# Optimization experiments

Measured on AMD Instinct MI355X. Metric: run time of the kernel, lower is better.

## Reference

```python
import jax, jax.numpy as jnp
import numpy as np

B, N, C = 2, 30, 320
FH = FW = 64          # feature map (latent 128 / downsample 2)
PH = PW = 32          # roi_scale output size at this level
ORIG = 128.0          # original (latent) spatial size
SCALE = 0.5           # spatial_scale = 1/downsample_rate
SR = 2                # sampling_ratio
M = N + 1             # global channel + rois


def _bilinear(img, y, x):
    # img: (C, H, W); y, x: arbitrary-shape float coords. torchvision-style:
    # zero outside [-1, H]/[ -1, W], clamp then 4-corner interp.
    H, W = img.shape[1], img.shape[2]
    valid = (y > -1.0) & (y < H) & (x > -1.0) & (x < W)
    yc = jnp.clip(y, 0.0, H - 1.0)
    xc = jnp.clip(x, 0.0, W - 1.0)
    y0 = jnp.floor(yc).astype(jnp.int32)
    x0 = jnp.floor(xc).astype(jnp.int32)
    y1 = jnp.minimum(y0 + 1, H - 1)
    x1 = jnp.minimum(x0 + 1, W - 1)
    wy = yc - y0
    wx = xc - x0
    v = (img[:, y0, x0] * (1 - wy) * (1 - wx)
         + img[:, y0, x1] * (1 - wy) * wx
         + img[:, y1, x0] * wy * (1 - wx)
         + img[:, y1, x1] * wy * wx)
    return v * valid


def _roi_align_one(img, x1, y1, bw, bh):
    # img (C,FH,FW); x1,y1,bw,bh (N,) in aligned feature coords / bin sizes
    s = (jnp.arange(PH * SR, dtype=img.dtype) + 0.5) / SR   # sub-sample offsets in bin units
    yy = y1[:, None] + s[None, :] * bh[:, None]             # (N, PH*SR)
    xx = x1[:, None] + s[None, :] * bw[:, None]             # (N, PW*SR)
    yg = jnp.broadcast_to(yy[:, :, None], (N, PH * SR, PW * SR))
    xg = jnp.broadcast_to(xx[:, None, :], (N, PH * SR, PW * SR))
    v = _bilinear(img, yg, xg)                              # (C, N, PH*SR, PW*SR)
    v = v.reshape(C, N, PH, SR, PW, SR).mean(axis=(3, 5))   # average sub-samples
    return v.transpose(1, 0, 2, 3)                          # (N, C, PH, PW)


def _roi_unpool_one(roi_imgs, x1, y1, bw, bh):
    # inverse of roi_align: paste each (C,PH,PW) roi back into its own (FH,FW) map
    ys = jnp.arange(FH, dtype=roi_imgs.dtype)
    xs = jnp.arange(FW, dtype=roi_imgs.dtype)
    ry = (ys[None, :] - y1[:, None]) / bh[:, None] - 0.5    # (N, FH) roi-grid coords
    rx = (xs[None, :] - x1[:, None]) / bw[:, None] - 0.5    # (N, FW)
    ryg = jnp.broadcast_to(ry[:, :, None], (N, FH, FW))
    rxg = jnp.broadcast_to(rx[:, None, :], (N, FH, FW))
    return jax.vmap(_bilinear)(roi_imgs, ryg, rxg)          # (N, C, FH, FW); zeros outside box


def _fuser(x, perm, w_reduce, w1, b1, w2, b2):
    # FuseWeightGenerator: x (B, M, C, H, W)
    fg = jnp.sum(x, axis=2) != 0                            # (B, M, H, W) foreground mask
    fw = jnp.einsum('bmchw,c->bmhw', x, w_reduce)           # 1x1 conv C->1, no bias
    g = fw[:, :1]
    r = fw[:, 1:][:, perm]                                  # shuffle roi channels
    gin = jnp.concatenate([g, r], axis=1)                   # (B, M, H, W)
    # ChannelGate: only the 'max' branch affects the output (original uses last channel_att_raw)
    mp = gin.max(axis=(2, 3))                               # (B, M)
    att = jax.nn.relu(mp @ w1 + b1) @ w2 + b2
    gated = gin * jax.nn.sigmoid(att)[:, :, None, None]
    inv = jnp.argsort(perm)
    fw = jnp.concatenate([gated[:, :1], gated[:, 1:][:, inv]], axis=1)
    fw = jnp.where(fg, fw, jnp.finfo(fw.dtype).min)
    w = jax.nn.softmax(fw, axis=1)[:, :, None]              # (B, M, 1, H, W)
    return jnp.sum(x * w, axis=1)                           # (B, C, H, W)


def _forward(normed_hidden_states, attn_output, instance_boxes, instance_masks, perm,
             w_reduce, w1, b1, w2, b2):
    fmap = normed_hidden_states.reshape(B, FH, FW, C).transpose(0, 3, 1, 2)  # b c h w
    boxes = instance_boxes * ORIG * SCALE - 0.5             # aligned=True feature coords
    x1, y1 = boxes[..., 0], boxes[..., 1]
    x2, y2 = boxes[..., 2], boxes[..., 3]
    bw = (x2 - x1) / PW
    bh = (y2 - y1) / PH
    roi_feats = jax.vmap(_roi_align_one)(fmap, x1, y1, bw, bh)   # (B,N,C,PH,PW)
    mask = instance_masks.astype(roi_feats.dtype)[:, :, None, None, None]
    roi_feats = roi_feats * mask                             # masked rois stay zero
    unpooled = jax.vmap(_roi_unpool_one)(roi_feats, x1, y1, bw, bh) * mask  # (B,N,C,FH,FW)
    attn_map = attn_output.reshape(B, FH, FW, C).transpose(0, 3, 1, 2)[:, None]
    x = jnp.concatenate([attn_map, unpooled], axis=1)        # (B, M, C, FH, FW)
    fused = _fuser(x, perm, w_reduce, w1, b1, w2, b2)        # (B, C, FH, FW)
    return fused.transpose(0, 2, 3, 1).reshape(B, FH * FW, C)


def setup_inputs() -> dict:
    key = jax.random.key(0)
    ks = jax.random.split(key, 10)
    nhs = jax.random.normal(ks[0], (B, FH * FW, C), dtype=jnp.float32)
    attn = jax.random.normal(ks[1], (B, FH * FW, C), dtype=jnp.float32)
    cx = jax.random.uniform(ks[2], (B, N), minval=0.25, maxval=0.75)
    cy = jax.random.uniform(ks[3], (B, N), minval=0.25, maxval=0.75)
    hw = jax.random.uniform(ks[4], (B, N, 2), minval=0.1, maxval=0.4)
    boxes = jnp.stack([cx - hw[..., 0] / 2, cy - hw[..., 1] / 2,
                       cx + hw[..., 0] / 2, cy + hw[..., 1] / 2], axis=-1)
    boxes = jnp.clip(boxes, 0.0, 1.0).astype(jnp.float32)    # normalized xyxy
    masks = jax.random.randint(ks[5], (B, N), 0, 2).astype(jnp.int32)
    perm = jax.random.permutation(ks[6], N).astype(jnp.int32)
    w_reduce = (jax.random.normal(ks[7], (C,), dtype=jnp.float32) / np.sqrt(C)).astype(jnp.float32)
    w1 = (jax.random.normal(ks[8], (M, M), dtype=jnp.float32) / np.sqrt(M)).astype(jnp.float32)
    b1 = jnp.zeros((M,), dtype=jnp.float32)
    w2 = (jax.random.normal(ks[9], (M, M), dtype=jnp.float32) / np.sqrt(M)).astype(jnp.float32)
    b2 = jnp.zeros((M,), dtype=jnp.float32)
    return {"normed_hidden_states": nhs, "attn_output": attn, "instance_boxes": boxes,
            "instance_masks": masks, "perm": perm, "w_reduce": w_reduce,
            "w1": w1, "b1": b1, "w2": w2, "b2": b2}


def reference(normed_hidden_states, attn_output, instance_boxes, instance_masks, perm,
              w_reduce, w1, b1, w2, b2):
    return _forward(normed_hidden_states, attn_output, instance_boxes, instance_masks, perm,
                    w_reduce, w1, b1, w2, b2)
```

## Files before the change

kernel.cpp:

```cpp
#include <hip/hip_runtime.h>
#include <hip/hip_bf16.h>

#define NB 2
#define NN 30
#define NC 320
#define NM 31
#define HW 4096
#define FMIN_F (-3.40282346638528859812e+38f)

typedef float nfloat4 __attribute__((ext_vector_type(4)));

#define OFF_FSUM   0
#define OFF_FWRED  8192
#define OFF_ASUM   16384
#define OFF_AWRED  24576
#define OFF_Z      32768
#define OFF_MP     286720
#define WS_FLOATS  286784

#define GRID_ROIF (NB * NN * 256)
#define GRID_RED  1639

__device__ __forceinline__ void get_box(const float* boxes, int b, int n,
                                        float& x1, float& y1, float& bw, float& bh) {
    const float* p = boxes + (b * NN + n) * 4;
    float X1 = p[0] * 64.0f - 0.5f;
    float Y1 = p[1] * 64.0f - 0.5f;
    float X2 = p[2] * 64.0f - 0.5f;
    float Y2 = p[3] * 64.0f - 0.5f;
    x1 = X1; y1 = Y1;
    bw = (X2 - X1) / 32.0f;
    bh = (Y2 - Y1) / 32.0f;
}

__device__ __forceinline__ unsigned short f2bf(float f) {
    __hip_bfloat16 h = __float2bfloat16(f);
    return *reinterpret_cast<unsigned short*>(&h);
}
__device__ __forceinline__ float bf2f(unsigned short u) {
    return __uint_as_float(((unsigned int)u) << 16);
}

__device__ void do_roifeat(int blk, const float* __restrict__ nhs,
                           const float* __restrict__ boxes,
                           const int* __restrict__ masks,
                           unsigned short* __restrict__ roif) {
    int bn = blk >> 8;
    int n = bn % NN;
    int b = bn / NN;
    if (masks[b * NN + n] == 0) return;
    int tid = threadIdx.x;
    int cid = tid / 80;
    int v = tid - cid * 80;
    int cell = blk * 4 + cid;
    int q = cell & 31;
    int p = (cell >> 5) & 31;
    float x1, y1, bw, bh;
    get_box(boxes, b, n, x1, y1, bw, bh);
    float wc[4][4];
    int ic[4][4];
    bool vv[4];
#pragma unroll
    for (int s_ = 0; s_ < 4; s_++) {
        int di = s_ >> 1, dj = s_ & 1;
        float y = y1 + ((float)p + 0.25f + 0.5f * (float)di) * bh;
        float x = x1 + ((float)q + 0.25f + 0.5f * (float)dj) * bw;
        vv[s_] = (y > -1.0f) && (y < 64.0f) && (x > -1.0f) && (x < 64.0f);
        float yc = fminf(fmaxf(y, 0.0f), 63.0f);
        float xc = fminf(fmaxf(x, 0.0f), 63.0f);
        int iy0 = (int)floorf(yc), ix0 = (int)floorf(xc);
        int iy1 = min(iy0 + 1, 63), ix1 = min(ix0 + 1, 63);
        float wy = yc - (float)iy0, wx = xc - (float)ix0;
        wc[s_][0] = (1.f - wy) * (1.f - wx);
        wc[s_][1] = (1.f - wy) * wx;
        wc[s_][2] = wy * (1.f - wx);
        wc[s_][3] = wy * wx;
        ic[s_][0] = iy0 * 64 + ix0;
        ic[s_][1] = iy0 * 64 + ix1;
        ic[s_][2] = iy1 * 64 + ix0;
        ic[s_][3] = iy1 * 64 + ix1;
    }
    const float4* fb4 = (const float4*)(nhs + (size_t)b * HW * NC);
    float4 acc = make_float4(0.f, 0.f, 0.f, 0.f);
#pragma unroll
    for (int s_ = 0; s_ < 4; s_++) {
        if (vv[s_]) {
#pragma unroll
            for (int t_ = 0; t_ < 4; t_++) {
                float w = wc[s_][t_];
                float4 fv = fb4[ic[s_][t_] * 80 + v];
                acc.x += w * fv.x; acc.y += w * fv.y;
                acc.z += w * fv.z; acc.w += w * fv.w;
            }
        }
    }
    ushort4 pk;
    pk.x = f2bf(acc.x * 0.25f);
    pk.y = f2bf(acc.y * 0.25f);
    pk.z = f2bf(acc.z * 0.25f);
    pk.w = f2bf(acc.w * 0.25f);
    ((ushort4*)roif)[(size_t)cell * 80 + v] = pk;
}

__device__ void do_reduce(int rblk, const float* __restrict__ nhs,
                          const float* __restrict__ attn,
                          const float* __restrict__ wred, float* __restrict__ ws) {
    int wave = threadIdx.x >> 6;
    int lane = threadIdx.x & 63;
    int row = rblk * 5 + wave;
    if (row >= NB * HW) return;
    const float4* n4 = (const float4*)(nhs + (size_t)row * NC);
    const float4* a4 = (const float4*)(attn + (size_t)row * NC);
    const float4* w4 = (const float4*)wred;
    float4 wv = w4[lane];
    float4 nv = n4[lane];
    float4 av = a4[lane];
    float s_n = nv.x + nv.y + nv.z + nv.w;
    float w_n = nv.x * wv.x + nv.y * wv.y + nv.z * wv.z + nv.w * wv.w;
    float s_a = av.x + av.y + av.z + av.w;
    float w_a = av.x * wv.x + av.y * wv.y + av.z * wv.z + av.w * wv.w;
    if (lane < 16) {
        float4 wv2 = w4[lane + 64];
        float4 nv2 = n4[lane + 64];
        float4 av2 = a4[lane + 64];
        s_n += nv2.x + nv2.y + nv2.z + nv2.w;
        w_n += nv2.x * wv2.x + nv2.y * wv2.y + nv2.z * wv2.z + nv2.w * wv2.w;
        s_a += av2.x + av2.y + av2.z + av2.w;
        w_a += av2.x * wv2.x + av2.y * wv2.y + av2.z * wv2.z + av2.w * wv2.w;
    }
#pragma unroll
    for (int off = 32; off > 0; off >>= 1) {
        s_n += __shfl_down(s_n, off, 64);
        w_n += __shfl_down(w_n, off, 64);
        s_a += __shfl_down(s_a, off, 64);
        w_a += __shfl_down(w_a, off, 64);
    }
    if (lane == 0) {
        ws[OFF_FSUM + row]  = s_n;
        ws[OFF_FWRED + row] = w_n;
        ws[OFF_ASUM + row]  = s_a;
        ws[OFF_AWRED + row] = w_a;
    }
}

__global__ void k_stage1(const float* __restrict__ nhs, const float* __restrict__ attn,
                         const float* __restrict__ boxes, const int* __restrict__ masks,
                         const float* __restrict__ wred, float* __restrict__ ws,
                         unsigned short* __restrict__ roif) {
    int blk = blockIdx.x;
    if (blk < GRID_ROIF) {
        do_roifeat(blk, nhs, boxes, masks, roif);
    } else {
        do_reduce(blk - GRID_ROIF, nhs, attn, wred, ws);
    }
}

__global__ void k_fw(const float* __restrict__ boxes, const int* __restrict__ masks,
                     float* __restrict__ ws) {
    int bm = blockIdx.x;
    int b = bm / NM, m = bm % NM;
    __shared__ float rs[1024], rw[1024];
    __shared__ float red[256];
    float locmax = -INFINITY;
    int tid = threadIdx.x;
    if (m == 0) {
        for (int pix = tid; pix < HW; pix += 256) {
            float fwv = ws[OFF_AWRED + b * HW + pix];
            bool fg = (ws[OFF_ASUM + b * HW + pix] != 0.0f);
            ws[OFF_Z + (size_t)bm * HW + pix] = fg ? fwv : FMIN_F;
            locmax = fmaxf(locmax, fwv);
        }
    } else {
        int n = m - 1;
        int msk = masks[b * NN + n];
        if (msk) {
            float x1, y1, bw, bh;
            get_box(boxes, b, n, x1, y1, bw, bh);
            const float* fsum  = ws + OFF_FSUM + b * HW;
            const float* fwred = ws + OFF_FWRED + b * HW;
            for (int cell = tid; cell < 1024; cell += 256) {
                int q = cell & 31, p = cell >> 5;
                float accs = 0.f, accw = 0.f;
#pragma unroll
                for (int di = 0; di < 2; di++) {
#pragma unroll
                    for (int dj = 0; dj < 2; dj++) {
                        float y = y1 + ((float)p + 0.25f + 0.5f * (float)di) * bh;
                        float x = x1 + ((float)q + 0.25f + 0.5f * (float)dj) * bw;
                        bool valid = (y > -1.0f) && (y < 64.0f) && (x > -1.0f) && (x < 64.0f);
                        if (valid) {
                            float yc = fminf(fmaxf(y, 0.0f), 63.0f);
                            float xc = fminf(fmaxf(x, 0.0f), 63.0f);
                            int iy0 = (int)floorf(yc), ix0 = (int)floorf(xc);
                            int iy1 = min(iy0 + 1, 63), ix1 = min(ix0 + 1, 63);
                            float wy = yc - (float)iy0, wx = xc - (float)ix0;
                            float w00 = (1.f - wy) * (1.f - wx), w01 = (1.f - wy) * wx;
                            float w10 = wy * (1.f - wx), w11 = wy * wx;
                            accs += w00 * fsum[iy0 * 64 + ix0] + w01 * fsum[iy0 * 64 + ix1]
                                  + w10 * fsum[iy1 * 64 + ix0] + w11 * fsum[iy1 * 64 + ix1];
                            accw += w00 * fwred[iy0 * 64 + ix0] + w01 * fwred[iy0 * 64 + ix1]
                                  + w10 * fwred[iy1 * 64 + ix0] + w11 * fwred[iy1 * 64 + ix1];
                        }
                    }
                }
                rs[cell] = accs * 0.25f;
                rw[cell] = accw * 0.25f;
            }
            __syncthreads();
            for (int pix = tid; pix < HW; pix += 256) {
                int h = pix >> 6, wp = pix & 63;
                float fwv = 0.0f;
                bool fg = false;
                float ry = ((float)h - y1) / bh - 0.5f;
                float rx = ((float)wp - x1) / bw - 0.5f;
                bool valid = (ry > -1.0f) && (ry < 32.0f) && (rx > -1.0f) && (rx < 32.0f);
                if (valid) {
                    float yc = fminf(fmaxf(ry, 0.0f), 31.0f);
                    float xc = fminf(fmaxf(rx, 0.0f), 31.0f);
                    int iy0 = (int)floorf(yc), ix0 = (int)floorf(xc);
                    int iy1 = min(iy0 + 1, 31), ix1 = min(ix0 + 1, 31);
                    float wy = yc - (float)iy0, wx = xc - (float)ix0;
                    float w00 = (1.f - wy) * (1.f - wx), w01 = (1.f - wy) * wx;
                    float w10 = wy * (1.f - wx), w11 = wy * wx;
                    fwv = w00 * rw[iy0 * 32 + ix0] + w01 * rw[iy0 * 32 + ix1]
                        + w10 * rw[iy1 * 32 + ix0] + w11 * rw[iy1 * 32 + ix1];
                    float su = w00 * rs[iy0 * 32 + ix0] + w01 * rs[iy0 * 32 + ix1]
                             + w10 * rs[iy1 * 32 + ix0] + w11 * rs[iy1 * 32 + ix1];
                    fg = (su != 0.0f);
                }
                ws[OFF_Z + (size_t)bm * HW + pix] = fg ? fwv : FMIN_F;
                locmax = fmaxf(locmax, fwv);
            }
        } else {
            for (int pix = tid; pix < HW; pix += 256)
                ws[OFF_Z + (size_t)bm * HW + pix] = FMIN_F;
            locmax = 0.0f;
        }
    }
    red[tid] = locmax;
    __syncthreads();
    for (int s = 128; s > 0; s >>= 1) {
        if (tid < s) red[tid] = fmaxf(red[tid], red[tid + s]);
        __syncthreads();
    }
    if (tid == 0) ws[OFF_MP + bm] = red[0];
}

__global__ void k_final(const float* __restrict__ attn, const float* __restrict__ boxes,
                        const int* __restrict__ perm, const float* __restrict__ w1,
                        const float* __restrict__ b1, const float* __restrict__ w2,
                        const float* __restrict__ b2, const float* __restrict__ ws,
                        const unsigned short* __restrict__ roif, float* __restrict__ out) {
    __shared__ float mpg[NM], hb[NM], scal[32], wbuf[4][32];
    int t = threadIdx.x;
    int idx0 = blockIdx.x * 4;
    int b = idx0 >> 12;

    if (t < NM) {
        mpg[t] = (t == 0) ? ws[OFF_MP + b * NM]
                          : ws[OFF_MP + b * NM + 1 + perm[t - 1]];
    }
    __syncthreads();
    if (t < NM) {
        float a = b1[t];
#pragma unroll
        for (int k = 0; k < NM; k++) a += mpg[k] * w1[k * NM + t];
        hb[t] = fmaxf(a, 0.0f);
    }
    __syncthreads();
    if (t < NM) {
        float a = b2[t];
#pragma unroll
        for (int k = 0; k < NM; k++) a += hb[k] * w2[k * NM + t];
        float sig = 1.0f / (1.0f + expf(-a));
        if (t == 0) scal[0] = sig;
        else        scal[1 + perm[t - 1]] = sig;
    }
    __syncthreads();

    if (t < 128) {
        int pg = t >> 5, m = t & 31;
        int pix = (idx0 + pg) & 4095;
        float zz = FMIN_F;
        if (m < NM) {
            float v = ws[OFF_Z + (size_t)(b * NM + m) * HW + pix];
            zz = (v == FMIN_F) ? FMIN_F : v * scal[m];
        }
        float mx = zz;
#pragma unroll
        for (int off = 16; off > 0; off >>= 1)
            mx = fmaxf(mx, __shfl_xor(mx, off, 64));
        float e = (m < NM) ? expf(zz - mx) : 0.0f;
        float s = e;
#pragma unroll
        for (int off = 16; off > 0; off >>= 1)
            s += __shfl_xor(s, off, 64);
        if (m < NM) wbuf[pg][m] = e / s;
    }
    __syncthreads();

    int pid = t / 80;
    int v = t - pid * 80;
    int idx = idx0 + pid;
    int pix = idx & 4095;
    int h = pix >> 6, wp = pix & 63;
    float w0 = wbuf[pid][0];
    float4 a4 = ((const float4*)attn)[(size_t)idx * 80 + v];
    float4 acc;
    acc.x = a4.x * w0; acc.y = a4.y * w0; acc.z = a4.z * w0; acc.w = a4.w * w0;
    const ushort4* r4 = (const ushort4*)roif;
    for (int n = 0; n < NN; n++) {
        float wn = wbuf[pid][n + 1];
        if (wn == 0.0f) continue;
        float x1, y1, bw, bh;
        get_box(boxes, b, n, x1, y1, bw, bh);
        float ry = ((float)h - y1) / bh - 0.5f;
        float rx = ((float)wp - x1) / bw - 0.5f;
        float yc = fminf(fmaxf(ry, 0.0f), 31.0f);
        float xc = fminf(fmaxf(rx, 0.0f), 31.0f);
        int iy0 = (int)floorf(yc), ix0 = (int)floorf(xc);
        int iy1 = min(iy0 + 1, 31), ix1 = min(ix0 + 1, 31);
        float wy = yc - (float)iy0, wx = xc - (float)ix0;
        float w00 = (1.f - wy) * (1.f - wx) * wn, w01 = (1.f - wy) * wx * wn;
        float w10 = wy * (1.f - wx) * wn, w11 = wy * wx * wn;
        size_t base = ((size_t)(b * NN + n)) << 10;
        ushort4 u00 = r4[(base + iy0 * 32 + ix0) * 80 + v];
        ushort4 u01 = r4[(base + iy0 * 32 + ix1) * 80 + v];
        ushort4 u10 = r4[(base + iy1 * 32 + ix0) * 80 + v];
        ushort4 u11 = r4[(base + iy1 * 32 + ix1) * 80 + v];
        acc.x += w00 * bf2f(u00.x) + w01 * bf2f(u01.x) + w10 * bf2f(u10.x) + w11 * bf2f(u11.x);
        acc.y += w00 * bf2f(u00.y) + w01 * bf2f(u01.y) + w10 * bf2f(u10.y) + w11 * bf2f(u11.y);
        acc.z += w00 * bf2f(u00.z) + w01 * bf2f(u01.z) + w10 * bf2f(u10.z) + w11 * bf2f(u11.z);
        acc.w += w00 * bf2f(u00.w) + w01 * bf2f(u01.w) + w10 * bf2f(u10.w) + w11 * bf2f(u11.w);
    }
    nfloat4 nv = { acc.x, acc.y, acc.z, acc.w };
    __builtin_nontemporal_store(nv, ((nfloat4*)out) + (size_t)idx * 80 + v);
}

extern "C" void kernel_launch(void* const* d_in, const int* in_sizes, int n_in,
                              void* d_out, int out_size, void* d_ws, size_t ws_size,
                              hipStream_t stream) {
    const float* nhs   = (const float*)d_in[0];
    const float* attn  = (const float*)d_in[1];
    const float* boxes = (const float*)d_in[2];
    const int*   masks = (const int*)d_in[3];
    const int*   perm  = (const int*)d_in[4];
    const float* wred  = (const float*)d_in[5];
    const float* w1    = (const float*)d_in[6];
    const float* b1    = (const float*)d_in[7];
    const float* w2    = (const float*)d_in[8];
    const float* b2    = (const float*)d_in[9];
    float* out = (float*)d_out;
    float* ws = (float*)d_ws;
    unsigned short* roif = (unsigned short*)((char*)d_ws + (size_t)WS_FLOATS * 4);

    k_stage1<<<GRID_ROIF + GRID_RED, 320, 0, stream>>>(nhs, attn, boxes, masks, wred, ws, roif);
    k_fw<<<NB * NM, 256, 0, stream>>>(boxes, masks, ws);
    k_final<<<NB * HW / 4, 320, 0, stream>>>(attn, boxes, perm, w1, b1, w2, b2, ws, roif, out);
}
```

Baseline: 131.6 us.

## Merge ROI-align subsample taps into a 3x3 footprint and widen per-thread vectors

ROI feature pooling now computes, once per cell in shared memory, a combined 3x3 weight stencil covering all four subsamples. Each cell's channels are then gathered once per distinct pixel instead of up to sixteen times. Both the ROI-feature pass and the final kernel now process 8 channels per thread using 128-bit bf16 packs, with 8 pixels per block, which halves the block count. The out-of-range validity checks are dropped in the ROI and k_fw sampling. This relies on boxes being clipped to [0,1] and on subsample spacing staying within one pixel.

```diff
diff --git a/kernel.cpp b/kernel.cpp
--- a/kernel.cpp
+++ b/kernel.cpp
@@ -18,7 +18,7 @@
 #define OFF_MP     286720
 #define WS_FLOATS  286784
 
-#define GRID_ROIF (NB * NN * 256)
+#define GRID_ROIF (NB * NN * 128)
 #define GRID_RED  1639
 
 __device__ __forceinline__ void get_box(const float* boxes, int b, int n,
@@ -37,69 +37,103 @@
     __hip_bfloat16 h = __float2bfloat16(f);
     return *reinterpret_cast<unsigned short*>(&h);
 }
-__device__ __forceinline__ float bf2f(unsigned short u) {
-    return __uint_as_float(((unsigned int)u) << 16);
-}
+__device__ __forceinline__ unsigned pack2(float a, float b) {
+    return (unsigned)f2bf(a) | ((unsigned)f2bf(b) << 16);
+}
+__device__ __forceinline__ float blo(unsigned u) { return __uint_as_float(u << 16); }
+__device__ __forceinline__ float bhi(unsigned u) { return __uint_as_float(u & 0xffff0000u); }
 
 __device__ void do_roifeat(int blk, const float* __restrict__ nhs,
                            const float* __restrict__ boxes,
                            const int* __restrict__ masks,
-                           unsigned short* __restrict__ roif) {
-    int bn = blk >> 8;
+                           unsigned* __restrict__ roif) {
+    int bn = blk >> 7;
     int n = bn % NN;
     int b = bn / NN;
     if (masks[b * NN + n] == 0) return;
+    __shared__ float wsm[8][9];
+    __shared__ int bsm[8];
     int tid = threadIdx.x;
-    int cid = tid / 80;
-    int v = tid - cid * 80;
-    int cell = blk * 4 + cid;
-    int q = cell & 31;
-    int p = (cell >> 5) & 31;
     float x1, y1, bw, bh;
     get_box(boxes, b, n, x1, y1, bw, bh);
-    float wc[4][4];
-    int ic[4][4];
-    bool vv[4];
-#pragma unroll
-    for (int s_ = 0; s_ < 4; s_++) {
-        int di = s_ >> 1, dj = s_ & 1;
-        float y = y1 + ((float)p + 0.25f + 0.5f * (float)di) * bh;
-        float x = x1 + ((float)q + 0.25f + 0.5f * (float)dj) * bw;
-        vv[s_] = (y > -1.0f) && (y < 64.0f) && (x > -1.0f) && (x < 64.0f);
-        float yc = fminf(fmaxf(y, 0.0f), 63.0f);
-        float xc = fminf(fmaxf(x, 0.0f), 63.0f);
-        int iy0 = (int)floorf(yc), ix0 = (int)floorf(xc);
-        int iy1 = min(iy0 + 1, 63), ix1 = min(ix0 + 1, 63);
-        float wy = yc - (float)iy0, wx = xc - (float)ix0;
-        wc[s_][0] = (1.f - wy) * (1.f - wx);
-        wc[s_][1] = (1.f - wy) * wx;
-        wc[s_][2] = wy * (1.f - wx);
-        wc[s_][3] = wy * wx;
-        ic[s_][0] = iy0 * 64 + ix0;
-        ic[s_][1] = iy0 * 64 + ix1;
-        ic[s_][2] = iy1 * 64 + ix0;
-        ic[s_][3] = iy1 * 64 + ix1;
-    }
+
+    if (tid < 8) {
+        int cell = blk * 8 + tid;
+        int q = cell & 31;
+        int p = (cell >> 5) & 31;
+        float W[9] = {0.f,0.f,0.f,0.f,0.f,0.f,0.f,0.f,0.f};
+        float wys[4], wxs[4];
+        int iy0s[4], ix0s[4];
+        int iymin = 64, ixmin = 64;
+#pragma unroll
+        for (int s_ = 0; s_ < 4; s_++) {
+            int di = s_ >> 1, dj = s_ & 1;
+            float y = y1 + ((float)p + 0.25f + 0.5f * (float)di) * bh;
+            float x = x1 + ((float)q + 0.25f + 0.5f * (float)dj) * bw;
+            float yc = fminf(fmaxf(y, 0.0f), 63.0f);
+            float xc = fminf(fmaxf(x, 0.0f), 63.0f);
+            int iy0 = (int)floorf(yc), ix0 = (int)floorf(xc);
+            wys[s_] = yc - (float)iy0;
+            wxs[s_] = xc - (float)ix0;
+            iy0s[s_] = iy0; ix0s[s_] = ix0;
+            iymin = min(iymin, iy0); ixmin = min(ixmin, ix0);
+        }
+#pragma unroll
+        for (int s_ = 0; s_ < 4; s_++) {
+            float wy = wys[s_], wx = wxs[s_];
+            int dy = iy0s[s_] - iymin;
+            int dx = ix0s[s_] - ixmin;
+            bool yt = (iy0s[s_] == 63);
+            bool xt = (ix0s[s_] == 63);
+            float ay0 = yt ? 1.0f : (1.0f - wy);
+            float ay1 = yt ? 0.0f : wy;
+            float ax0 = xt ? 1.0f : (1.0f - wx);
+            float ax1 = xt ? 0.0f : wx;
+            float r0 = dy ? 0.0f : ay0;
+            float r1 = dy ? ay0  : ay1;
+            float r2 = dy ? ay1  : 0.0f;
+            float c0 = dx ? 0.0f : ax0;
+            float c1 = dx ? ax0  : ax1;
+            float c2 = dx ? ax1  : 0.0f;
+            W[0] += r0 * c0; W[1] += r0 * c1; W[2] += r0 * c2;
+            W[3] += r1 * c0; W[4] += r1 * c1; W[5] += r1 * c2;
+            W[6] += r2 * c0; W[7] += r2 * c1; W[8] += r2 * c2;
+        }
+#pragma unroll
+        for (int k = 0; k < 9; k++) wsm[tid][k] = W[k] * 0.25f;
+        bsm[tid] = iymin * 64 + ixmin;
+    }
+    __syncthreads();
+
+    int cid = tid / 40;
+    int v = tid - cid * 40;
+    int cell = blk * 8 + cid;
     const float4* fb4 = (const float4*)(nhs + (size_t)b * HW * NC);
-    float4 acc = make_float4(0.f, 0.f, 0.f, 0.f);
-#pragma unroll
-    for (int s_ = 0; s_ < 4; s_++) {
-        if (vv[s_]) {
-#pragma unroll
-            for (int t_ = 0; t_ < 4; t_++) {
-                float w = wc[s_][t_];
-                float4 fv = fb4[ic[s_][t_] * 80 + v];
-                acc.x += w * fv.x; acc.y += w * fv.y;
-                acc.z += w * fv.z; acc.w += w * fv.w;
+    int base = bsm[cid];
+    float4 acc0 = make_float4(0.f, 0.f, 0.f, 0.f);
+    float4 acc1 = make_float4(0.f, 0.f, 0.f, 0.f);
+#pragma unroll
+    for (int i = 0; i < 3; i++) {
+#pragma unroll
+        for (int j = 0; j < 3; j++) {
+            float w = wsm[cid][i * 3 + j];
+            if (w != 0.0f) {
+                int off = (base + i * 64 + j) * 80 + v * 2;
+                float4 f0 = fb4[off];
+                float4 f1 = fb4[off + 1];
+                acc0.x += w * f0.x; acc0.y += w * f0.y;
+                acc0.z += w * f0.z; acc0.w += w * f0.w;
+                acc1.x += w * f1.x; acc1.y += w * f1.y;
+                acc1.z += w * f1.z; acc1.w += w * f1.w;
             }
         }
     }
-    ushort4 pk;
-    pk.x = f2bf(acc.x * 0.25f);
-    pk.y = f2bf(acc.y * 0.25f);
-    pk.z = f2bf(acc.z * 0.25f);
-    pk.w = f2bf(acc.w * 0.25f);
-    ((ushort4*)roif)[(size_t)cell * 80 + v] = pk;
+    uint4 pk;
+    pk.x = pack2(acc0.x, acc0.y);
+    pk.y = pack2(acc0.z, acc0.w);
+    pk.z = pack2(acc1.x, acc1.y);
+    pk.w = pack2(acc1.z, acc1.w);
+    ((uint4*)roif)[(size_t)cell * 40 + v] = pk;
 }
 
 __device__ void do_reduce(int rblk, const float* __restrict__ nhs,
@@ -146,7 +180,7 @@
 __global__ void k_stage1(const float* __restrict__ nhs, const float* __restrict__ attn,
                          const float* __restrict__ boxes, const int* __restrict__ masks,
                          const float* __restrict__ wred, float* __restrict__ ws,
-                         unsigned short* __restrict__ roif) {
+                         unsigned* __restrict__ roif) {
     int blk = blockIdx.x;
     if (blk < GRID_ROIF) {
         do_roifeat(blk, nhs, boxes, masks, roif);
@@ -187,20 +221,17 @@
                     for (int dj = 0; dj < 2; dj++) {
                         float y = y1 + ((float)p + 0.25f + 0.5f * (float)di) * bh;
                         float x = x1 + ((float)q + 0.25f + 0.5f * (float)dj) * bw;
-                        bool valid = (y > -1.0f) && (y < 64.0f) && (x > -1.0f) && (x < 64.0f);
-                        if (valid) {
-                            float yc = fminf(fmaxf(y, 0.0f), 63.0f);
-                            float xc = fminf(fmaxf(x, 0.0f), 63.0f);
-                            int iy0 = (int)floorf(yc), ix0 = (int)floorf(xc);
-                            int iy1 = min(iy0 + 1, 63), ix1 = min(ix0 + 1, 63);
-                            float wy = yc - (float)iy0, wx = xc - (float)ix0;
-                            float w00 = (1.f - wy) * (1.f - wx), w01 = (1.f - wy) * wx;
-                            float w10 = wy * (1.f - wx), w11 = wy * wx;
-                            accs += w00 * fsum[iy0 * 64 + ix0] + w01 * fsum[iy0 * 64 + ix1]
-                                  + w10 * fsum[iy1 * 64 + ix0] + w11 * fsum[iy1 * 64 + ix1];
-                            accw += w00 * fwred[iy0 * 64 + ix0] + w01 * fwred[iy0 * 64 + ix1]
-                                  + w10 * fwred[iy1 * 64 + ix0] + w11 * fwred[iy1 * 64 + ix1];
-                        }
+                        float yc = fminf(fmaxf(y, 0.0f), 63.0f);
+                        float xc = fminf(fmaxf(x, 0.0f), 63.0f);
+                        int iy0 = (int)floorf(yc), ix0 = (int)floorf(xc);
+                        int iy1 = min(iy0 + 1, 63), ix1 = min(ix0 + 1, 63);
+                        float wy = yc - (float)iy0, wx = xc - (float)ix0;
+                        float w00 = (1.f - wy) * (1.f - wx), w01 = (1.f - wy) * wx;
+                        float w10 = wy * (1.f - wx), w11 = wy * wx;
+                        accs += w00 * fsum[iy0 * 64 + ix0] + w01 * fsum[iy0 * 64 + ix1]
+                              + w10 * fsum[iy1 * 64 + ix0] + w11 * fsum[iy1 * 64 + ix1];
+                        accw += w00 * fwred[iy0 * 64 + ix0] + w01 * fwred[iy0 * 64 + ix1]
+                              + w10 * fwred[iy1 * 64 + ix0] + w11 * fwred[iy1 * 64 + ix1];
                     }
                 }
                 rs[cell] = accs * 0.25f;
@@ -250,10 +281,10 @@
                         const int* __restrict__ perm, const float* __restrict__ w1,
                         const float* __restrict__ b1, const float* __restrict__ w2,
                         const float* __restrict__ b2, const float* __restrict__ ws,
-                        const unsigned short* __restrict__ roif, float* __restrict__ out) {
-    __shared__ float mpg[NM], hb[NM], scal[32], wbuf[4][32];
+                        const unsigned* __restrict__ roif, float* __restrict__ out) {
+    __shared__ float mpg[NM], hb[NM], scal[32], wbuf[8][32];
     int t = threadIdx.x;
-    int idx0 = blockIdx.x * 4;
+    int idx0 = blockIdx.x * 8;
     int b = idx0 >> 12;
 
     if (t < NM) {
@@ -278,7 +309,7 @@
     }
     __syncthreads();
 
-    if (t < 128) {
+    if (t < 256) {
         int pg = t >> 5, m = t & 31;
         int pix = (idx0 + pg) & 4095;
         float zz = FMIN_F;
@@ -299,16 +330,19 @@
     }
     __syncthreads();
 
-    int pid = t / 80;
-    int v = t - pid * 80;
+    int pid = t / 40;
+    int v = t - pid * 40;
     int idx = idx0 + pid;
     int pix = idx & 4095;
     int h = pix >> 6, wp = pix & 63;
     float w0 = wbuf[pid][0];
-    float4 a4 = ((const float4*)attn)[(size_t)idx * 80 + v];
-    float4 acc;
-    acc.x = a4.x * w0; acc.y = a4.y * w0; acc.z = a4.z * w0; acc.w = a4.w * w0;
-    const ushort4* r4 = (const ushort4*)roif;
+    const float4* at4 = (const float4*)attn;
+    float4 a0 = at4[(size_t)idx * 80 + v * 2];
+    float4 a1 = at4[(size_t)idx * 80 + v * 2 + 1];
+    float4 acc0, acc1;
+    acc0.x = a0.x * w0; acc0.y = a0.y * w0; acc0.z = a0.z * w0; acc0.w = a0.w * w0;
+    acc1.x = a1.x * w0; acc1.y = a1.y * w0; acc1.z = a1.z * w0; acc1.w = a1.w * w0;
+    const uint4* r4 = (const uint4*)roif;
     for (int n = 0; n < NN; n++) {
         float wn = wbuf[pid][n + 1];
         if (wn == 0.0f) continue;
@@ -324,17 +358,23 @@
         float w00 = (1.f - wy) * (1.f - wx) * wn, w01 = (1.f - wy) * wx * wn;
         float w10 = wy * (1.f - wx) * wn, w11 = wy * wx * wn;
         size_t base = ((size_t)(b * NN + n)) << 10;
-        ushort4 u00 = r4[(base + iy0 * 32 + ix0) * 80 + v];
-        ushort4 u01 = r4[(base + iy0 * 32 + ix1) * 80 + v];
-        ushort4 u10 = r4[(base + iy1 * 32 + ix0) * 80 + v];
-        ushort4 u11 = r4[(base + iy1 * 32 + ix1) * 80 + v];
-        acc.x += w00 * bf2f(u00.x) + w01 * bf2f(u01.x) + w10 * bf2f(u10.x) + w11 * bf2f(u11.x);
-        acc.y += w00 * bf2f(u00.y) + w01 * bf2f(u01.y) + w10 * bf2f(u10.y) + w11 * bf2f(u11.y);
-        acc.z += w00 * bf2f(u00.z) + w01 * bf2f(u01.z) + w10 * bf2f(u10.z) + w11 * bf2f(u11.z);
-        acc.w += w00 * bf2f(u00.w) + w01 * bf2f(u01.w) + w10 * bf2f(u10.w) + w11 * bf2f(u11.w);
-    }
-    nfloat4 nv = { acc.x, acc.y, acc.z, acc.w };
-    __builtin_nontemporal_store(nv, ((nfloat4*)out) + (size_t)idx * 80 + v);
+        uint4 U00 = r4[(base + iy0 * 32 + ix0) * 40 + v];
+        uint4 U01 = r4[(base + iy0 * 32 + ix1) * 40 + v];
+        uint4 U10 = r4[(base + iy1 * 32 + ix0) * 40 + v];
+        uint4 U11 = r4[(base + iy1 * 32 + ix1) * 40 + v];
+        acc0.x += w00 * blo(U00.x) + w01 * blo(U01.x) + w10 * blo(U10.x) + w11 * blo(U11.x);
+        acc0.y += w00 * bhi(U00.x) + w01 * bhi(U01.x) + w10 * bhi(U10.x) + w11 * bhi(U11.x);
+        acc0.z += w00 * blo(U00.y) + w01 * blo(U01.y) + w10 * blo(U10.y) + w11 * blo(U11.y);
+        acc0.w += w00 * bhi(U00.y) + w01 * bhi(U01.y) + w10 * bhi(U10.y) + w11 * bhi(U11.y);
+        acc1.x += w00 * blo(U00.z) + w01 * blo(U01.z) + w10 * blo(U10.z) + w11 * blo(U11.z);
+        acc1.y += w00 * bhi(U00.z) + w01 * bhi(U01.z) + w10 * bhi(U10.z) + w11 * bhi(U11.z);
+        acc1.z += w00 * blo(U00.w) + w01 * blo(U01.w) + w10 * blo(U10.w) + w11 * blo(U11.w);
+        acc1.w += w00 * bhi(U00.w) + w01 * bhi(U01.w) + w10 * bhi(U10.w) + w11 * bhi(U11.w);
+    }
+    nfloat4 nv0 = { acc0.x, acc0.y, acc0.z, acc0.w };
+    nfloat4 nv1 = { acc1.x, acc1.y, acc1.z, acc1.w };
+    __builtin_nontemporal_store(nv0, ((nfloat4*)out) + (size_t)idx * 80 + v * 2);
+    __builtin_nontemporal_store(nv1, ((nfloat4*)out) + (size_t)idx * 80 + v * 2 + 1);
 }
 
 extern "C" void kernel_launch(void* const* d_in, const int* in_sizes, int n_in,
@@ -352,9 +392,9 @@
     const float* b2    = (const float*)d_in[9];
     float* out = (float*)d_out;
     float* ws = (float*)d_ws;
-    unsigned short* roif = (unsigned short*)((char*)d_ws + (size_t)WS_FLOATS * 4);
+    unsigned* roif = (unsigned*)((char*)d_ws + (size_t)WS_FLOATS * 4);
 
     k_stage1<<<GRID_ROIF + GRID_RED, 320, 0, stream>>>(nhs, attn, boxes, masks, wred, ws, roif);
     k_fw<<<NB * NM, 256, 0, stream>>>(boxes, masks, ws);
-    k_final<<<NB * HW / 4, 320, 0, stream>>>(attn, boxes, perm, w1, b1, w2, b2, ws, roif, out);
-}
+    k_final<<<NB * HW / 8, 320, 0, stream>>>(attn, boxes, perm, w1, b1, w2, b2, ws, roif, out);
+}
```

After: 119.7 us. 1.1x faster.
